# Kernel optimization log

Hardware: AMD Instinct MI355X
Metric: run time of the kernel (lower is better)

## Reference

```python
import jax, jax.numpy as jnp
import numpy as np

B, S, E, H = 2, 2048, 1024, 16
D = E // H  # head_dim = 64

def setup_inputs() -> dict:
    key = jax.random.key(0)
    k1, k2, k3 = jax.random.split(key, 3)
    x = jax.random.normal(k1, (B, S, E), dtype=jnp.float32)
    W_attn = jax.random.normal(k2, (E, 3 * E), dtype=jnp.float32) * 0.02
    b_attn = jnp.zeros((3 * E,), dtype=jnp.float32)
    W_proj = jax.random.normal(k3, (E, E), dtype=jnp.float32) * 0.02
    b_proj = jnp.zeros((E,), dtype=jnp.float32)
    return {"x": x, "W_attn": W_attn, "b_attn": b_attn, "W_proj": W_proj, "b_proj": b_proj}

def reference(x, W_attn, b_attn, W_proj, b_proj):
    bsz, seq, emb = x.shape
    # fused QKV projection (Conv1D == linear with [in,out] weight)
    qkv = x @ W_attn + b_attn                       # [B,S,3E]
    q, k, v = jnp.split(qkv, 3, axis=-1)
    def to_heads(t):
        return t.reshape(bsz, seq, H, D).transpose(0, 2, 1, 3)  # [B,H,S,D]
    q, k, v = to_heads(q), to_heads(k), to_heads(v)
    scale = jnp.float32(D) ** -0.5
    scores = jnp.einsum('bhqd,bhkd->bhqk', q, k) * scale        # [B,H,S,S]
    causal = jnp.tril(jnp.ones((seq, seq), dtype=bool))
    scores = jnp.where(causal, scores, jnp.float32(-jnp.inf))
    attn = jax.nn.softmax(scores, axis=-1)
    out = jnp.einsum('bhqk,bhkd->bhqd', attn, v)                # [B,H,S,D]
    out = out.transpose(0, 2, 1, 3).reshape(bsz, seq, emb)
    y = out @ W_proj + b_proj
    return y
```

## Files before the change

kernel.cpp:

```cpp
#include <hip/hip_runtime.h>
#include <hip/hip_bf16.h>


typedef __bf16 bf16;
typedef __bf16 bf16x4 __attribute__((ext_vector_type(4)));
typedef __bf16 bf16x8 __attribute__((ext_vector_type(8)));
typedef float  f32x4  __attribute__((ext_vector_type(4)));

#define MNEG (-1.0e30f)
#define QSCALE 0.1803368801f

__device__ __forceinline__ void gload16(const bf16* g, bf16* l) {
  __builtin_amdgcn_global_load_lds((const __attribute__((address_space(1))) void*)g,
                                   (__attribute__((address_space(3))) void*)l, 16, 0, 0);
}

__global__ __launch_bounds__(256) void prep_k(const float* __restrict__ x, bf16* __restrict__ xb,
                                              const float* __restrict__ Wa, bf16* __restrict__ WaT,
                                              const float* __restrict__ Wp, bf16* __restrict__ WpT) {
  const int bid = blockIdx.x;
  if (bid < 2048) {
    const int i = bid * 256 + threadIdx.x;
    f32x4 a = ((const f32x4*)x)[2 * i], b = ((const f32x4*)x)[2 * i + 1];
    bf16x8 o;
    for (int j = 0; j < 4; ++j) { o[j] = (bf16)a[j]; o[4 + j] = (bf16)b[j]; }
    ((bf16x8*)xb)[i] = o;
    return;
  }
  __shared__ bf16 t[64][68];
  const float* in; bf16* out; int C, cx, cy;
  if (bid < 2816) { in = Wa; out = WaT; C = 3072; const int tt = bid - 2048; cx = tt % 48; cy = tt / 48; }
  else            { in = Wp; out = WpT; C = 1024; const int tt = bid - 2816; cx = tt % 16; cy = tt / 16; }
  const int R = 1024;
  const int c0 = cx * 64, r0 = cy * 64;
  const int lr = threadIdx.x >> 4;
  const int lc = (threadIdx.x & 15) * 4;
  for (int i = 0; i < 4; ++i) {
    int r = lr + i * 16;
    f32x4 v = *(const f32x4*)(in + (size_t)(r0 + r) * C + c0 + lc);
    bf16x4 b;
    for (int j = 0; j < 4; ++j) b[j] = (bf16)v[j];
    *(bf16x4*)&t[r][lc] = b;
  }
  __syncthreads();
  for (int i = 0; i < 4; ++i) {
    int c = lr + i * 16;
    bf16x4 v;
    for (int j = 0; j < 4; ++j) v[j] = t[lc + j][c];
    *(bf16x4*)(out + (size_t)(c0 + c) * R + r0 + lc) = v;
  }
}

template <int MODE, int BN>
__global__ __launch_bounds__(512) void gemm_bt(const bf16* __restrict__ A,
                                               const bf16* __restrict__ Bt,
                                               const float* __restrict__ bias,
                                               float* __restrict__ C,
                                               bf16* __restrict__ Qo,
                                               bf16* __restrict__ Ko,
                                               bf16* __restrict__ Vo,
                                               int M, int N, int K) {
  constexpr int WN = BN / 32;
  constexpr int WM = 8 / WN;
  constexpr int MR = 128 / WM;
  constexpr int MT = MR / 16;
  __shared__ bf16 As0[128 * 32], As1[128 * 32];
  __shared__ bf16 Bs0[BN * 32],  Bs1[BN * 32];
  const int tid = threadIdx.x;
  const int w = tid >> 6, l = tid & 63;
  const int nx = gridDim.x;
  const int nwg = nx * gridDim.y;
  const int flat = blockIdx.y * nx + blockIdx.x;
  const int swz = (flat & 7) * (nwg >> 3) + (flat >> 3);
  const int m0 = (swz / nx) * 128, n0 = (swz % nx) * BN;
  const int wm = w / WN, wn = w % WN;
  const int fr = l & 15, fg = l >> 4;
  const int grow = tid >> 2;
  const int gcol = (tid & 3) * 8;

  f32x4 acc[MT][2] = {};

  for (int k0 = 0; k0 < K; k0 += 64) {
    __syncthreads();
    gload16(A + (size_t)(m0 + grow) * K + k0 + gcol,      As0 + 512 * w);
    gload16(A + (size_t)(m0 + grow) * K + k0 + 32 + gcol, As1 + 512 * w);
    if (BN == 128 || w < 4) {
      gload16(Bt + (size_t)(n0 + grow) * K + k0 + gcol,      Bs0 + 512 * w);
      gload16(Bt + (size_t)(n0 + grow) * K + k0 + 32 + gcol, Bs1 + 512 * w);
    }
    __syncthreads();

    bf16x8 af[MT][2], bfv[2][2];
    for (int mt = 0; mt < MT; ++mt) {
      af[mt][0] = *(const bf16x8*)(As0 + (wm * MR + mt * 16 + fr) * 32 + 8 * fg);
      af[mt][1] = *(const bf16x8*)(As1 + (wm * MR + mt * 16 + fr) * 32 + 8 * fg);
    }
    for (int nt = 0; nt < 2; ++nt) {
      bfv[nt][0] = *(const bf16x8*)(Bs0 + (wn * 32 + nt * 16 + fr) * 32 + 8 * fg);
      bfv[nt][1] = *(const bf16x8*)(Bs1 + (wn * 32 + nt * 16 + fr) * 32 + 8 * fg);
    }
    for (int mt = 0; mt < MT; ++mt)
      for (int nt = 0; nt < 2; ++nt) {
        acc[mt][nt] = __builtin_amdgcn_mfma_f32_16x16x32_bf16(af[mt][0], bfv[nt][0], acc[mt][nt], 0, 0, 0);
        acc[mt][nt] = __builtin_amdgcn_mfma_f32_16x16x32_bf16(af[mt][1], bfv[nt][1], acc[mt][nt], 0, 0, 0);
      }
  }

  for (int mt = 0; mt < MT; ++mt) {
    for (int nt = 0; nt < 2; ++nt) {
      const int row0 = m0 + wm * MR + mt * 16 + 4 * fg;
      const int col = n0 + wn * 32 + nt * 16 + fr;
      const float bv = bias[col];
      if (MODE == 0) {
        for (int r = 0; r < 4; ++r)
          C[(size_t)(row0 + r) * N + col] = acc[mt][nt][r] + bv;
      } else {
        const int which = col >> 10, h = (col >> 6) & 15, d = col & 63;
        const int b = row0 >> 11, s = row0 & 2047;
        if (which == 2) {
          bf16x4 vv;
          for (int r = 0; r < 4; ++r) vv[r] = (bf16)(acc[mt][nt][r] + bv);
          *(bf16x4*)(Vo + ((size_t)(b * 16 + h) * 64 + d) * 2048 + s) = vv;
        } else if (which == 0) {
          for (int r = 0; r < 4; ++r)
            Qo[((size_t)(b * 16 + h) * 2048 + s + r) * 64 + d] =
                (bf16)((acc[mt][nt][r] + bv) * QSCALE);
        } else {
          for (int r = 0; r < 4; ++r)
            Ko[((size_t)(b * 16 + h) * 2048 + s + r) * 64 + d] = (bf16)(acc[mt][nt][r] + bv);
        }
      }
    }
  }
}

__global__ __launch_bounds__(256, 3) void attn_k(const bf16* __restrict__ Qw,
                                                 const bf16* __restrict__ Kw,
                                                 const bf16* __restrict__ VtG,
                                                 bf16* __restrict__ AO) {
  __shared__ bf16 Ks[128 * 72];
  __shared__ bf16 Vt[64 * 136];
  __shared__ bf16 Ps[4 * 16 * 72];
  const int tid = threadIdx.x, w = tid >> 6, l = tid & 63;
  const int bid = blockIdx.x;
  const int bh = ((bid & 7) << 2) | ((bid >> 3) & 3);
  const int qt = 31 - (bid >> 5);
  const int q0 = qt * 64;
  const int fr = l & 15, fg = l >> 4;
  const size_t base = (size_t)bh * 2048 * 64;
  const int qw0 = q0 + w * 16;
  const int q = qw0 + fr;
  bf16* Pw = Ps + w * 16 * 72;
  const int r8 = tid >> 3, c8 = (tid & 7) * 8;
  const int r16 = tid >> 4, c16 = (tid & 15) * 8;

  bf16x8 qf[2];
  for (int t = 0; t < 2; ++t)
    qf[t] = *(const bf16x8*)(Qw + base + (size_t)(qw0 + fr) * 64 + 32 * t + 8 * fg);

  f32x4 oacc[4] = {};
  float lsum = 0.f;
  bf16x8 kreg[4], vreg[4];

  auto load_tile = [&](int kt) {
    for (int c = 0; c < 4; ++c) {
      kreg[c] = *(const bf16x8*)(Kw + base + (size_t)(kt + r8 + 32 * c) * 64 + c8);
      vreg[c] = *(const bf16x8*)(VtG + base + (size_t)(r16 + 16 * c) * 2048 + kt + c16);
    }
  };
  auto write_tile = [&]() {
    for (int c = 0; c < 4; ++c) {
      *(bf16x8*)(Ks + (r8 + 32 * c) * 72 + c8) = kreg[c];
      *(bf16x8*)(Vt + (r16 + 16 * c) * 136 + c16) = vreg[c];
    }
  };

  load_tile(0);
  write_tile();
  __syncthreads();

  for (int kt = 0; kt <= q0; kt += 128) {
    const bool havenext = (kt + 128 <= q0);
    if (havenext) load_tile(kt + 128);

    for (int h = 0; h < 2; ++h) {
      const int kh = kt + 64 * h;
      if (kh > q0) break;

      f32x4 sc[4];
      __builtin_amdgcn_s_setprio(1);
      for (int c = 0; c < 4; ++c) {
        bf16x8 kf0 = *(const bf16x8*)(Ks + (64 * h + c * 16 + fr) * 72 + 8 * fg);
        bf16x8 kf1 = *(const bf16x8*)(Ks + (64 * h + c * 16 + fr) * 72 + 32 + 8 * fg);
        f32x4 z = {};
        z = __builtin_amdgcn_mfma_f32_16x16x32_bf16(kf0, qf[0], z, 0, 0, 0);
        sc[c] = __builtin_amdgcn_mfma_f32_16x16x32_bf16(kf1, qf[1], z, 0, 0, 0);
      }
      __builtin_amdgcn_s_setprio(0);

      const bool need_mask = (kh + 63 > qw0);
      float psum = 0.f;
      for (int c = 0; c < 4; ++c) {
        bf16x4 pb;
        for (int r = 0; r < 4; ++r) {
          float s = sc[c][r];
          if (need_mask && (kh + c * 16 + 4 * fg + r > q)) s = MNEG;
          const float pv = __builtin_amdgcn_exp2f(s);
          psum += pv;
          pb[r] = (bf16)pv;
        }
        *(bf16x4*)(Pw + fr * 72 + c * 16 + 4 * fg) = pb;
      }
      psum += __shfl_xor(psum, 16, 64);
      psum += __shfl_xor(psum, 32, 64);
      lsum += psum;

      asm volatile("" ::: "memory");
      __builtin_amdgcn_s_setprio(1);
      for (int t = 0; t < 2; ++t) {
        bf16x8 pa = *(const bf16x8*)(Pw + fr * 72 + 32 * t + 8 * fg);
        for (int dt = 0; dt < 4; ++dt) {
          bf16x8 vf = *(const bf16x8*)(Vt + (dt * 16 + fr) * 136 + 64 * h + 32 * t + 8 * fg);
          oacc[dt] = __builtin_amdgcn_mfma_f32_16x16x32_bf16(pa, vf, oacc[dt], 0, 0, 0);
        }
      }
      __builtin_amdgcn_s_setprio(0);
      asm volatile("" ::: "memory");
    }

    if (!havenext) break;
    __syncthreads();
    write_tile();
    __syncthreads();
  }

  const int b = bh >> 4, h = bh & 15;
  float linv[4];
  for (int r = 0; r < 4; ++r)
    linv[r] = 1.f / __shfl(lsum, (l & 48) | (4 * fg + r), 64);
  for (int dt = 0; dt < 4; ++dt)
    for (int r = 0; r < 4; ++r) {
      const int qq = qw0 + 4 * fg + r;
      AO[(size_t)(b * 2048 + qq) * 1024 + h * 64 + dt * 16 + fr] =
          (bf16)(oacc[dt][r] * linv[r]);
    }
}

extern "C" void kernel_launch(void* const* d_in, const int* in_sizes, int n_in,
                              void* d_out, int out_size, void* d_ws, size_t ws_size,
                              hipStream_t stream) {
  const float* x      = (const float*)d_in[0];
  const float* W_attn = (const float*)d_in[1];
  const float* b_attn = (const float*)d_in[2];
  const float* W_proj = (const float*)d_in[3];
  const float* b_proj = (const float*)d_in[4];
  float* out = (float*)d_out;

  char* ws = (char*)d_ws;
  bf16* WaT = (bf16*)(ws);
  bf16* WpT = (bf16*)(ws + 6291456);
  bf16* Qw  = (bf16*)(ws + 8388608);
  bf16* Kw  = (bf16*)(ws + 16777216);
  bf16* VtG = (bf16*)(ws + 25165824);
  bf16* AO  = (bf16*)(ws + 33554432);
  bf16* xb  = AO;

  prep_k<<<3072, 256, 0, stream>>>(x, xb, W_attn, WaT, W_proj, WpT);

  gemm_bt<1, 128><<<dim3(24, 32), 512, 0, stream>>>(
      xb, WaT, b_attn, nullptr, Qw, Kw, VtG, 4096, 3072, 1024);

  attn_k<<<1024, 256, 0, stream>>>(Qw, Kw, VtG, AO);

  gemm_bt<0, 64><<<dim3(16, 32), 512, 0, stream>>>(
      AO, WpT, b_proj, out, nullptr, nullptr, nullptr, 4096, 1024, 1024);
}
```

Measured before the change: 109.4 us.

## Double-buffer GEMM LDS tiles and prefetch next K-slice during MFMA

The bf16 GEMM kernel now keeps two LDS buffers for the A and B tiles. It issues the asynchronous global-to-LDS loads for the next K-slice before running the MFMAs on the current slice, which replaces the two barriers per iteration with one. It also raises wave priority around the MFMA block with s_setprio. The intent is to hide global load latency behind matrix math. In exchange, LDS use per workgroup doubles, which can lower occupancy.

Result: slower. 115.0 us (+5.2%).

```diff
diff --git a/kernel.cpp b/kernel.cpp
--- a/kernel.cpp
+++ b/kernel.cpp
@@ -64,8 +64,8 @@
   constexpr int WM = 8 / WN;
   constexpr int MR = 128 / WM;
   constexpr int MT = MR / 16;
-  __shared__ bf16 As0[128 * 32], As1[128 * 32];
-  __shared__ bf16 Bs0[BN * 32],  Bs1[BN * 32];
+  __shared__ bf16 As[2][2][128 * 32];
+  __shared__ bf16 Bs[2][2][BN * 32];
   const int tid = threadIdx.x;
   const int w = tid >> 6, l = tid & 63;
   const int nx = gridDim.x;
@@ -80,30 +80,46 @@
 
   f32x4 acc[MT][2] = {};
 
+  auto stage = [&](int k0, int buf) {
+    gload16(A + (size_t)(m0 + grow) * K + k0 + gcol,      As[buf][0] + 512 * w);
+    gload16(A + (size_t)(m0 + grow) * K + k0 + 32 + gcol, As[buf][1] + 512 * w);
+    if (BN == 128 || w < 4) {
+      gload16(Bt + (size_t)(n0 + grow) * K + k0 + gcol,      Bs[buf][0] + 512 * w);
+      gload16(Bt + (size_t)(n0 + grow) * K + k0 + 32 + gcol, Bs[buf][1] + 512 * w);
+    }
+  };
+
+  stage(0, 0);
+  __syncthreads();
+
+  int cur = 0;
   for (int k0 = 0; k0 < K; k0 += 64) {
-    __syncthreads();
-    gload16(A + (size_t)(m0 + grow) * K + k0 + gcol,      As0 + 512 * w);
-    gload16(A + (size_t)(m0 + grow) * K + k0 + 32 + gcol, As1 + 512 * w);
-    if (BN == 128 || w < 4) {
-      gload16(Bt + (size_t)(n0 + grow) * K + k0 + gcol,      Bs0 + 512 * w);
-      gload16(Bt + (size_t)(n0 + grow) * K + k0 + 32 + gcol, Bs1 + 512 * w);
-    }
-    __syncthreads();
+    if (k0 + 64 < K) stage(k0 + 64, cur ^ 1);
+
+    const bf16* as0 = As[cur][0];
+    const bf16* as1 = As[cur][1];
+    const bf16* bs0 = Bs[cur][0];
+    const bf16* bs1 = Bs[cur][1];
 
     bf16x8 af[MT][2], bfv[2][2];
     for (int mt = 0; mt < MT; ++mt) {
-      af[mt][0] = *(const bf16x8*)(As0 + (wm * MR + mt * 16 + fr) * 32 + 8 * fg);
-      af[mt][1] = *(const bf16x8*)(As1 + (wm * MR + mt * 16 + fr) * 32 + 8 * fg);
+      af[mt][0] = *(const bf16x8*)(as0 + (wm * MR + mt * 16 + fr) * 32 + 8 * fg);
+      af[mt][1] = *(const bf16x8*)(as1 + (wm * MR + mt * 16 + fr) * 32 + 8 * fg);
     }
     for (int nt = 0; nt < 2; ++nt) {
-      bfv[nt][0] = *(const bf16x8*)(Bs0 + (wn * 32 + nt * 16 + fr) * 32 + 8 * fg);
-      bfv[nt][1] = *(const bf16x8*)(Bs1 + (wn * 32 + nt * 16 + fr) * 32 + 8 * fg);
-    }
+      bfv[nt][0] = *(const bf16x8*)(bs0 + (wn * 32 + nt * 16 + fr) * 32 + 8 * fg);
+      bfv[nt][1] = *(const bf16x8*)(bs1 + (wn * 32 + nt * 16 + fr) * 32 + 8 * fg);
+    }
+    __builtin_amdgcn_s_setprio(1);
     for (int mt = 0; mt < MT; ++mt)
       for (int nt = 0; nt < 2; ++nt) {
         acc[mt][nt] = __builtin_amdgcn_mfma_f32_16x16x32_bf16(af[mt][0], bfv[nt][0], acc[mt][nt], 0, 0, 0);
         acc[mt][nt] = __builtin_amdgcn_mfma_f32_16x16x32_bf16(af[mt][1], bfv[nt][1], acc[mt][nt], 0, 0, 0);
       }
+    __builtin_amdgcn_s_setprio(0);
+
+    __syncthreads();
+    cur ^= 1;
   }
 
   for (int mt = 0; mt < MT; ++mt) {
```

## Double-buffer QKV GEMM with prefetch of next K-slice during MFMA

Applied to the files above, without the earlier changes.

Splits the templated GEMM into separate QKV and projection kernels. The QKV GEMM now uses ping-pong LDS buffers with a K-step of 32, issuing the next slice's global-to-LDS loads before computing on the current one and waiting with explicit vmcnt counts. This is meant to hide global load latency behind MFMA work, which the previous load-sync-compute loop left exposed. In exchange it doubles the number of loop iterations and barriers per tile, and correctness depends on the hand-written waitcnt placement.

New measurement: 106.6 us. 2.6% less time.

```diff
diff --git a/kernel.cpp b/kernel.cpp
--- a/kernel.cpp
+++ b/kernel.cpp
@@ -51,19 +51,92 @@
   }
 }
 
-template <int MODE, int BN>
-__global__ __launch_bounds__(512) void gemm_bt(const bf16* __restrict__ A,
-                                               const bf16* __restrict__ Bt,
-                                               const float* __restrict__ bias,
-                                               float* __restrict__ C,
-                                               bf16* __restrict__ Qo,
-                                               bf16* __restrict__ Ko,
-                                               bf16* __restrict__ Vo,
-                                               int M, int N, int K) {
-  constexpr int WN = BN / 32;
-  constexpr int WM = 8 / WN;
-  constexpr int MR = 128 / WM;
-  constexpr int MT = MR / 16;
+__global__ __launch_bounds__(512) void gemm_qkv(const bf16* __restrict__ A,
+                                                const bf16* __restrict__ Bt,
+                                                const float* __restrict__ bias,
+                                                bf16* __restrict__ Qo,
+                                                bf16* __restrict__ Ko,
+                                                bf16* __restrict__ Vo,
+                                                int M, int N, int K) {
+  __shared__ bf16 As[2][128 * 32];
+  __shared__ bf16 Bs[2][128 * 32];
+  const int tid = threadIdx.x;
+  const int w = tid >> 6, l = tid & 63;
+  const int nx = gridDim.x;
+  const int nwg = nx * gridDim.y;
+  const int flat = blockIdx.y * nx + blockIdx.x;
+  const int swz = (flat & 7) * (nwg >> 3) + (flat >> 3);
+  const int m0 = (swz / nx) * 128, n0 = (swz % nx) * 128;
+  const int wm = w >> 2, wn = w & 3;
+  const int fr = l & 15, fg = l >> 4;
+  const int grow = tid >> 2;
+  const int gcol = (tid & 3) * 8;
+
+  f32x4 acc[4][2] = {};
+
+  auto stage = [&](int k0, int buf) {
+    gload16(A  + (size_t)(m0 + grow) * K + k0 + gcol, As[buf] + 512 * w);
+    gload16(Bt + (size_t)(n0 + grow) * K + k0 + gcol, Bs[buf] + 512 * w);
+  };
+
+  stage(0, 0);
+
+  int cur = 0;
+  for (int k0 = 0; k0 < K; k0 += 32) {
+    const bool havenext = (k0 + 32 < K);
+    if (havenext) stage(k0 + 32, cur ^ 1);
+
+    if (havenext) asm volatile("s_waitcnt vmcnt(2)" ::: "memory");
+    else          asm volatile("s_waitcnt vmcnt(0)" ::: "memory");
+    __builtin_amdgcn_s_barrier();
+    asm volatile("" ::: "memory");
+
+    const bf16* as = As[cur];
+    const bf16* bs = Bs[cur];
+    bf16x8 af[4], bfv[2];
+    for (int mt = 0; mt < 4; ++mt)
+      af[mt] = *(const bf16x8*)(as + (wm * 64 + mt * 16 + fr) * 32 + 8 * fg);
+    for (int nt = 0; nt < 2; ++nt)
+      bfv[nt] = *(const bf16x8*)(bs + (wn * 32 + nt * 16 + fr) * 32 + 8 * fg);
+    for (int mt = 0; mt < 4; ++mt)
+      for (int nt = 0; nt < 2; ++nt)
+        acc[mt][nt] = __builtin_amdgcn_mfma_f32_16x16x32_bf16(af[mt], bfv[nt], acc[mt][nt], 0, 0, 0);
+
+    asm volatile("s_waitcnt lgkmcnt(0)" ::: "memory");
+    __builtin_amdgcn_sched_barrier(0);
+    __builtin_amdgcn_s_barrier();
+    cur ^= 1;
+  }
+
+  for (int mt = 0; mt < 4; ++mt) {
+    for (int nt = 0; nt < 2; ++nt) {
+      const int row0 = m0 + wm * 64 + mt * 16 + 4 * fg;
+      const int col = n0 + wn * 32 + nt * 16 + fr;
+      const float bv = bias[col];
+      const int which = col >> 10, h = (col >> 6) & 15, d = col & 63;
+      const int b = row0 >> 11, s = row0 & 2047;
+      if (which == 2) {
+        bf16x4 vv;
+        for (int r = 0; r < 4; ++r) vv[r] = (bf16)(acc[mt][nt][r] + bv);
+        *(bf16x4*)(Vo + ((size_t)(b * 16 + h) * 64 + d) * 2048 + s) = vv;
+      } else if (which == 0) {
+        for (int r = 0; r < 4; ++r)
+          Qo[((size_t)(b * 16 + h) * 2048 + s + r) * 64 + d] =
+              (bf16)((acc[mt][nt][r] + bv) * QSCALE);
+      } else {
+        for (int r = 0; r < 4; ++r)
+          Ko[((size_t)(b * 16 + h) * 2048 + s + r) * 64 + d] = (bf16)(acc[mt][nt][r] + bv);
+      }
+    }
+  }
+}
+
+__global__ __launch_bounds__(512) void gemm_proj(const bf16* __restrict__ A,
+                                                 const bf16* __restrict__ Bt,
+                                                 const float* __restrict__ bias,
+                                                 float* __restrict__ C,
+                                                 int M, int N, int K) {
+  constexpr int BN = 64, WN = 2, WM = 4, MR = 32, MT = 2;
   __shared__ bf16 As0[128 * 32], As1[128 * 32];
   __shared__ bf16 Bs0[BN * 32],  Bs1[BN * 32];
   const int tid = threadIdx.x;
@@ -84,7 +157,7 @@
     __syncthreads();
     gload16(A + (size_t)(m0 + grow) * K + k0 + gcol,      As0 + 512 * w);
     gload16(A + (size_t)(m0 + grow) * K + k0 + 32 + gcol, As1 + 512 * w);
-    if (BN == 128 || w < 4) {
+    if (w < 4) {
       gload16(Bt + (size_t)(n0 + grow) * K + k0 + gcol,      Bs0 + 512 * w);
       gload16(Bt + (size_t)(n0 + grow) * K + k0 + 32 + gcol, Bs1 + 512 * w);
     }
@@ -106,32 +179,14 @@
       }
   }
 
-  for (int mt = 0; mt < MT; ++mt) {
+  for (int mt = 0; mt < MT; ++mt)
     for (int nt = 0; nt < 2; ++nt) {
       const int row0 = m0 + wm * MR + mt * 16 + 4 * fg;
       const int col = n0 + wn * 32 + nt * 16 + fr;
       const float bv = bias[col];
-      if (MODE == 0) {
-        for (int r = 0; r < 4; ++r)
-          C[(size_t)(row0 + r) * N + col] = acc[mt][nt][r] + bv;
-      } else {
-        const int which = col >> 10, h = (col >> 6) & 15, d = col & 63;
-        const int b = row0 >> 11, s = row0 & 2047;
-        if (which == 2) {
-          bf16x4 vv;
-          for (int r = 0; r < 4; ++r) vv[r] = (bf16)(acc[mt][nt][r] + bv);
-          *(bf16x4*)(Vo + ((size_t)(b * 16 + h) * 64 + d) * 2048 + s) = vv;
-        } else if (which == 0) {
-          for (int r = 0; r < 4; ++r)
-            Qo[((size_t)(b * 16 + h) * 2048 + s + r) * 64 + d] =
-                (bf16)((acc[mt][nt][r] + bv) * QSCALE);
-        } else {
-          for (int r = 0; r < 4; ++r)
-            Ko[((size_t)(b * 16 + h) * 2048 + s + r) * 64 + d] = (bf16)(acc[mt][nt][r] + bv);
-        }
-      }
-    }
-  }
+      for (int r = 0; r < 4; ++r)
+        C[(size_t)(row0 + r) * N + col] = acc[mt][nt][r] + bv;
+    }
 }
 
 __global__ __launch_bounds__(256, 3) void attn_k(const bf16* __restrict__ Qw,
@@ -267,11 +322,11 @@
 
   prep_k<<<3072, 256, 0, stream>>>(x, xb, W_attn, WaT, W_proj, WpT);
 
-  gemm_bt<1, 128><<<dim3(24, 32), 512, 0, stream>>>(
-      xb, WaT, b_attn, nullptr, Qw, Kw, VtG, 4096, 3072, 1024);
+  gemm_qkv<<<dim3(24, 32), 512, 0, stream>>>(
+      xb, WaT, b_attn, Qw, Kw, VtG, 4096, 3072, 1024);
 
   attn_k<<<1024, 256, 0, stream>>>(Qw, Kw, VtG, AO);
 
-  gemm_bt<0, 64><<<dim3(16, 32), 512, 0, stream>>>(
-      AO, WpT, b_proj, out, nullptr, nullptr, nullptr, 4096, 1024, 1024);
-}
+  gemm_proj<<<dim3(16, 32), 512, 0, stream>>>(
+      AO, WpT, b_proj, out, 4096, 1024, 1024);
+}
```
